# Kernel optimization log

Hardware: AMD Instinct MI355X
Metric: run time of the kernel (lower is better)

The kernel has to match this reference:

```python
import jax, jax.numpy as jnp
import numpy as np

B, HH, WW, D, NH, DK, DV, RATIO = 16, 48, 48, 512, 8, 64, 64, 3
EPS = 1e-5

def setup_inputs() -> dict:
    key = jax.random.key(0)
    ks = jax.random.split(key, 12)
    nq = HH * WW
    w = lambda i, shape: jax.random.normal(ks[i], shape, jnp.float32) * 0.02
    return {
        "queries": jax.random.normal(ks[0], (B, nq, D), jnp.float32),
        "Wq": w(1, (D, NH * DK)), "bq": jnp.zeros((NH * DK,), jnp.float32),
        "Wk": w(2, (D, NH * DK)), "bk": jnp.zeros((NH * DK,), jnp.float32),
        "Wv": w(3, (D, NH * DV)), "bv": jnp.zeros((NH * DV,), jnp.float32),
        "Wo": w(4, (NH * DV, D)), "bo": jnp.zeros((D,), jnp.float32),
        "sr_w": w(5, (D, 1, RATIO + 1, RATIO + 1)),  # depthwise conv, OIHW with I=1
        "sr_b": jnp.zeros((D,), jnp.float32),
        "ln_g": jnp.ones((D,), jnp.float32), "ln_b": jnp.zeros((D,), jnp.float32),
        "tw": w(6, (NH, NH)),  # 1x1 conv over head dim
        "tb": jnp.zeros((NH,), jnp.float32),
    }


def reference(queries, Wq, bq, Wk, bk, Wv, bv, Wo, bo, sr_w, sr_b, ln_g, ln_b, tw, tb):
    b, nq, c = queries.shape
    # Q projection -> (b, h, nq, d_k)
    q = (queries @ Wq + bq).reshape(b, nq, NH, DK).transpose(0, 2, 1, 3)
    # spatial reduction: depthwise strided conv over (H, W)
    x = queries.transpose(0, 2, 1).reshape(b, c, HH, WW)
    pad = RATIO // 2
    x = jax.lax.conv_general_dilated(
        x, sr_w, window_strides=(RATIO, RATIO),
        padding=[(pad, pad), (pad, pad)], feature_group_count=c,
        dimension_numbers=("NCHW", "OIHW", "NCHW"))
    x = x + sr_b[None, :, None, None]
    nk = x.shape[2] * x.shape[3]
    x = x.reshape(b, c, nk).transpose(0, 2, 1)  # (b, nk, c)
    # LayerNorm over channel dim
    mu = x.mean(-1, keepdims=True)
    var = x.var(-1, keepdims=True)
    x = (x - mu) / jnp.sqrt(var + EPS) * ln_g + ln_b
    # K, V projections
    k = (x @ Wk + bk).reshape(b, nk, NH, DK).transpose(0, 2, 3, 1)  # (b,h,d_k,nk)
    v = (x @ Wv + bv).reshape(b, nk, NH, DV).transpose(0, 2, 1, 3)  # (b,h,nk,d_v)
    # scaled attention scores
    att = jnp.einsum("bhqd,bhdk->bhqk", q, k) / jnp.sqrt(jnp.float32(DK))
    # transform: 1x1 conv over heads -> softmax(-1) -> InstanceNorm2d (no affine)
    att = jnp.einsum("oi,biqk->boqk", tw, att) + tb[None, :, None, None]
    att = jax.nn.softmax(att, axis=-1)
    m = att.mean((2, 3), keepdims=True)
    va = att.var((2, 3), keepdims=True)
    att = (att - m) / jnp.sqrt(va + EPS)
    # apply to values and output projection
    out = jnp.einsum("bhqk,bhkd->bhqd", att, v).transpose(0, 2, 1, 3).reshape(b, nq, NH * DV)
    return out @ Wo + bo
```

## Files before the change

kernel.cpp:

```cpp
#include <hip/hip_runtime.h>
#include <hip/hip_bf16.h>
#include <stdint.h>


typedef __bf16 bf16;
typedef __bf16 bf16x4 __attribute__((ext_vector_type(4)));
typedef __bf16 bf16x8 __attribute__((ext_vector_type(8)));
typedef float  f32x4  __attribute__((ext_vector_type(4)));

#define LDS_AS  __attribute__((address_space(3)))
#define GLOB_AS __attribute__((address_space(1)))

__device__ __forceinline__ void gload_lds16(const bf16* g, void* l) {
    __builtin_amdgcn_global_load_lds((const GLOB_AS void*)g, (LDS_AS void*)l, 16, 0, 0);
}

#define NB   16
#define NQ   2304
#define DD   512
#define NKV  256

constexpr size_t OFF_WQT = 0;
constexpr size_t OFF_WKT = 512*512*2;
constexpr size_t OFF_WVT = 2*512*512*2;
constexpr size_t OFF_WOT = 3*512*512*2;
constexpr size_t OFF_X   = 4*512*512*2;
constexpr size_t OFF_KT  = OFF_X  + 4194304;
constexpr size_t OFF_VT  = OFF_KT + 4194304;
constexpr size_t OFF_SS  = OFF_VT + 4194304;
constexpr size_t OFF_SM  = OFF_SS + 512;
constexpr size_t OFF_TWF = OFF_SM + 24064;
constexpr size_t OFF_FLG = OFF_TWF + 256;
constexpr size_t OFF_QF  = OFF_FLG + 256;
constexpr size_t OFF_U   = OFF_QF + (size_t)NB*NQ*DD*2;
constexpr size_t OFF_S   = OFF_U  + (size_t)NB*NQ*DD*2;
constexpr size_t SPLANE  = (size_t)NQ*NKV*2;
constexpr size_t OFF_WOTP = OFF_X;

#define SM_BQ  0
#define SM_BK  512
#define SM_BV  1024
#define SM_BO  1536
#define SM_SRW 2048
#define SM_SRB 10240
#define SM_LNG 10752
#define SM_LNB 11264
#define SM_TW  11776

__global__ __launch_bounds__(64) void detect_dtype(const uint32_t* __restrict__ q,
                                                   int* __restrict__ flag)
{
    int t = threadIdx.x;
    int cnt = 0;
    #pragma unroll
    for (int i = 0; i < 8; i++) {
        uint32_t w = q[t*8 + i];
        int e = (w >> 7) & 0xFF;
        cnt += (e >= 100 && e <= 150) ? 1 : 0;
    }
    #pragma unroll
    for (int m = 1; m < 64; m <<= 1) cnt += __shfl_xor(cnt, m);
    if (t == 0) *flag = (cnt >= 384) ? 0 : 1;
}

__global__ __launch_bounds__(256) void convert_q(const void* __restrict__ in,
                                                 bf16* __restrict__ out,
                                                 const int* __restrict__ flag)
{
    if (*flag == 0) return;
    int idx = blockIdx.x * 256 + threadIdx.x;
    f32x4 a = ((const f32x4*)in)[(size_t)idx*2];
    f32x4 b = ((const f32x4*)in)[(size_t)idx*2 + 1];
    bf16x8 r;
    #pragma unroll
    for (int i = 0; i < 4; i++) { r[i] = (bf16)a[i]; r[i+4] = (bf16)b[i]; }
    ((bf16x8*)out)[idx] = r;
}

__global__ __launch_bounds__(256) void convert_small(
    const void* s0, const void* s1, const void* s2, const void* s3,
    const void* s4, const void* s5, const void* s6, const void* s7,
    const void* s8, bf16* __restrict__ dst, float* __restrict__ twf,
    const int* __restrict__ flag)
{
    const void* srcs[9] = {s0,s1,s2,s3,s4,s5,s6,s7,s8};
    const int sizes[9]  = {512,512,512,512,8192,512,512,512,64};
    const int offs[9]   = {SM_BQ,SM_BK,SM_BV,SM_BO,SM_SRW,SM_SRB,SM_LNG,SM_LNB,SM_TW};
    const float scl[9]  = {0.125f,1.f,1.f,1.f,1.f,1.f,1.f,1.f,1.f};
    int b = blockIdx.x;
    const void* s = srcs[b];
    int n = sizes[b], o = offs[b];
    float sc = scl[b];
    bool f32 = (*flag != 0);
    for (int i = threadIdx.x; i < n; i += 256) {
        float v = f32 ? ((const float*)s)[i] : (float)((const bf16*)s)[i];
        dst[o + i] = (bf16)(v * sc);
        if (b == 8) twf[i] = v;
    }
}

__global__ __launch_bounds__(256) void transpose512(
    const void* s0, const void* s1, const void* s2, const void* s3,
    bf16* __restrict__ d0, bf16* __restrict__ d1,
    bf16* __restrict__ d2, bf16* __restrict__ d3,
    const int* __restrict__ flag)
{
    __shared__ bf16 tile[32][33];
    bool f32 = (*flag != 0);
    int wsel = blockIdx.z;
    const void* src = wsel == 0 ? s0 : wsel == 1 ? s1 : wsel == 2 ? s2 : s3;
    bf16*       dst = wsel == 0 ? d0 : wsel == 1 ? d1 : wsel == 2 ? d2 : d3;
    float scl = (wsel == 0) ? 0.125f : 1.0f;
    int c0 = blockIdx.x * 32, n0 = blockIdx.y * 32;
    int tx = threadIdx.x, ty = threadIdx.y;
    #pragma unroll
    for (int i = 0; i < 4; i++) {
        size_t idx = (size_t)(c0 + ty + i*8) * 512 + n0 + tx;
        float v = f32 ? ((const float*)src)[idx] : (float)((const bf16*)src)[idx];
        tile[ty + i*8][tx] = (bf16)(v * scl);
    }
    __syncthreads();
    #pragma unroll
    for (int i = 0; i < 4; i++)
        dst[(size_t)(n0 + ty + i*8) * 512 + c0 + tx] = tile[tx][ty + i*8];
}

__global__ __launch_bounds__(256) void sr_ln(
    const void* __restrict__ qraw, const bf16* __restrict__ qc,
    const bf16* __restrict__ sm, bf16* __restrict__ x,
    const int* __restrict__ flag)
{
    const bf16* q = (*flag) ? qc : (const bf16*)qraw;
    const bf16* srw  = sm + SM_SRW;
    const bf16* srb  = sm + SM_SRB;
    const bf16* g    = sm + SM_LNG;
    const bf16* beta = sm + SM_LNB;
    int bo = blockIdx.x;
    int b  = bo >> 8, ok = bo & 255;
    int oh = ok >> 4, ow = ok & 15;
    int t  = threadIdx.x;

    float v[2];
    #pragma unroll
    for (int h = 0; h < 2; h++) {
        int ch = t + h*256;
        float acc = 0.f;
        #pragma unroll
        for (int kh = 0; kh < 4; kh++) {
            int ih = oh*3 - 1 + kh;
            if (ih < 0) continue;
            #pragma unroll
            for (int kw = 0; kw < 4; kw++) {
                int iw = ow*3 - 1 + kw;
                if (iw < 0) continue;
                acc += (float)q[((size_t)b*NQ + ih*48 + iw)*DD + ch]
                     * (float)srw[ch*16 + kh*4 + kw];
            }
        }
        v[h] = acc + (float)srb[ch];
    }
    float s = v[0] + v[1], s2 = v[0]*v[0] + v[1]*v[1];
    #pragma unroll
    for (int m = 1; m < 64; m <<= 1) { s += __shfl_xor(s, m); s2 += __shfl_xor(s2, m); }
    __shared__ float ps[4], ps2[4];
    if ((t & 63) == 0) { ps[t >> 6] = s; ps2[t >> 6] = s2; }
    __syncthreads();
    s  = ps[0] + ps[1] + ps[2] + ps[3];
    s2 = ps2[0] + ps2[1] + ps2[2] + ps2[3];
    float mu  = s * (1.f/512.f);
    float var = s2 * (1.f/512.f) - mu*mu;
    float inv = rsqrtf(var + 1e-5f);
    #pragma unroll
    for (int h = 0; h < 2; h++) {
        int ch = t + h*256;
        float y = (v[h] - mu) * inv * (float)g[ch] + (float)beta[ch];
        x[(size_t)bo * DD + ch] = (bf16)y;
    }
}

template <int MODE>
__global__ __launch_bounds__(256) void gemm_bt(
    const bf16* __restrict__ A, const bf16* __restrict__ Bt,
    const bf16* __restrict__ bias, bf16* __restrict__ C,
    const int* __restrict__ of32, const bf16* __restrict__ A2)
{
    constexpr int K = 512;
    __shared__ bf16 Al[128 * 64];
    __shared__ bf16 Bl[128 * 64];
    const int m0 = blockIdx.x * 128, n0 = blockIdx.y * 128;
    const int t = threadIdx.x;
    const int lane = t & 63, w = t >> 6;
    const int wr = w >> 1, wc = w & 1;
    const int gg = lane >> 4, li = lane & 15;
    const int fsw = (li & 7) << 4;
    bool f32o = false;
    if (MODE == 2) f32o = (*of32 != 0);

    const bf16* Ab = A;
    if (MODE == 4) Ab = (*of32) ? A2 : A;
    const bf16* Btb = Bt;
    if (MODE == 2) Btb = Bt + (size_t)(m0 / 2304) * (512 * 512);

    f32x4 acc[4][4] = {};

    for (int k0 = 0; k0 < K; k0 += 64) {
        #pragma unroll
        for (int p = 0; p < 4; p++) {
            int off = p*4096 + t*16;
            int row = off >> 7;
            int col = ((((off >> 4) & 7) ^ (row & 7)) << 3);
            gload_lds16(Ab + (size_t)(m0 + row)*K + k0 + col, (char*)Al + off);
        }
        #pragma unroll
        for (int p = 0; p < 4; p++) {
            int off = p*4096 + t*16;
            int row = off >> 7;
            int col = ((((off >> 4) & 7) ^ (row & 7)) << 3);
            gload_lds16(Btb + (size_t)(n0 + row)*K + k0 + col, (char*)Bl + off);
        }
        __syncthreads();
        #pragma unroll
        for (int kk = 0; kk < 2; kk++) {
            bf16x8 af[4], bfr[4];
            #pragma unroll
            for (int i = 0; i < 4; i++) {
                af[i]  = *(const bf16x8*)((char*)Al + (wr*64 + i*16 + li)*128 + ((kk*64 + gg*16) ^ fsw));
                bfr[i] = *(const bf16x8*)((char*)Bl + (wc*64 + i*16 + li)*128 + ((kk*64 + gg*16) ^ fsw));
            }
            __builtin_amdgcn_s_setprio(1);
            #pragma unroll
            for (int i = 0; i < 4; i++)
                #pragma unroll
                for (int j = 0; j < 4; j++)
                    acc[i][j] = __builtin_amdgcn_mfma_f32_16x16x32_bf16(af[i], bfr[j], acc[i][j], 0, 0, 0);
            __builtin_amdgcn_s_setprio(0);
        }
        __syncthreads();
    }

    #pragma unroll
    for (int i = 0; i < 4; i++) {
        #pragma unroll
        for (int j = 0; j < 4; j++) {
            int rbase = m0 + wr*64 + i*16 + gg*4;
            int c     = n0 + wc*64 + j*16 + li;
            float bv = (float)bias[c];
            #pragma unroll
            for (int jj = 0; jj < 4; jj++) {
                float val = acc[i][j][jj] + bv;
                int r = rbase + jj;
                if (MODE == 1) {
                    int bb = r >> 8, kk2 = r & 255;
                    int hh = c >> 6, dv = c & 63;
                    C[(((size_t)(bb*8 + hh))*64 + dv)*256 + kk2] = (bf16)val;
                } else if (MODE == 2) {
                    if (f32o) ((float*)C)[(size_t)r * 512 + c] = val;
                    else      C[(size_t)r * 512 + c] = (bf16)val;
                } else {
                    C[(size_t)r * 512 + c] = (bf16)val;
                }
            }
        }
    }
}

__global__ __launch_bounds__(256) void gemm_s(
    const bf16* __restrict__ Qf, const bf16* __restrict__ Kt, bf16* __restrict__ S,
    int b0)
{
    __shared__ bf16 Al[128 * 64];
    __shared__ bf16 Bl[128 * 64];
    const int m0 = blockIdx.x * 128, n0 = blockIdx.y * 128;
    const int bo = blockIdx.z;
    const int b = b0 + (bo >> 3), ih = bo & 7;
    const int t = threadIdx.x;
    const int lane = t & 63, w = t >> 6;
    const int wr = w >> 1, wc = w & 1;
    const int gg = lane >> 4, li = lane & 15;
    const int fsw = (li & 7) << 4;

    #pragma unroll
    for (int p = 0; p < 4; p++) {
        int off = p*4096 + t*16;
        int row = off >> 7;
        int col = ((((off >> 4) & 7) ^ (row & 7)) << 3);
        gload_lds16(Qf + ((size_t)(b*NQ + m0 + row))*DD + ih*64 + col, (char*)Al + off);
    }
    #pragma unroll
    for (int p = 0; p < 4; p++) {
        int off = p*4096 + t*16;
        int row = off >> 7;
        int col = ((((off >> 4) & 7) ^ (row & 7)) << 3);
        gload_lds16(Kt + ((size_t)(b*NKV + n0 + row))*DD + ih*64 + col, (char*)Bl + off);
    }
    __syncthreads();

    f32x4 acc[4][4] = {};
    #pragma unroll
    for (int kk = 0; kk < 2; kk++) {
        bf16x8 af[4], bfr[4];
        #pragma unroll
        for (int i = 0; i < 4; i++) {
            af[i]  = *(const bf16x8*)((char*)Al + (wr*64 + i*16 + li)*128 + ((kk*64 + gg*16) ^ fsw));
            bfr[i] = *(const bf16x8*)((char*)Bl + (wc*64 + i*16 + li)*128 + ((kk*64 + gg*16) ^ fsw));
        }
        __builtin_amdgcn_s_setprio(1);
        #pragma unroll
        for (int i = 0; i < 4; i++)
            #pragma unroll
            for (int j = 0; j < 4; j++)
                acc[i][j] = __builtin_amdgcn_mfma_f32_16x16x32_bf16(af[i], bfr[j], acc[i][j], 0, 0, 0);
        __builtin_amdgcn_s_setprio(0);
    }

    bf16* Sb = S + (size_t)bo * NQ * NKV;
    #pragma unroll
    for (int i = 0; i < 4; i++) {
        #pragma unroll
        for (int j = 0; j < 4; j++) {
            int rbase = m0 + wr*64 + i*16 + gg*4;
            int c     = n0 + wc*64 + j*16 + li;
            #pragma unroll
            for (int jj = 0; jj < 4; jj++)
                Sb[(size_t)(rbase + jj) * NKV + c] = (bf16)acc[i][j][jj];
        }
    }
}

__global__ __launch_bounds__(256) void mix_softmax(
    bf16* __restrict__ S, const float* __restrict__ twf,
    float* __restrict__ ssq_g, int b0)
{
    const int t = threadIdx.x;
    const int lane = t & 63, w = t >> 6;
    const int bl = blockIdx.y;
    const int b  = b0 + bl;
    const int q0 = blockIdx.x * 32 + w * 8;
    __shared__ float rpar[4][8];

    float tw[8][8];
    #pragma unroll
    for (int o = 0; o < 8; o++)
        #pragma unroll
        for (int i = 0; i < 8; i++)
            tw[o][i] = twf[o*8 + i];

    float ssqL[8] = {};
    for (int qi = 0; qi < 8; qi++) {
        float s[8][4];
        #pragma unroll
        for (int i = 0; i < 8; i++) {
            bf16x4 v = *(const bf16x4*)(S + (((size_t)(bl*8 + i))*NQ + (q0 + qi))*NKV + lane*4);
            #pragma unroll
            for (int r = 0; r < 4; r++) s[i][r] = (float)v[r];
        }
        float e[8][4], inv[8];
        #pragma unroll
        for (int o = 0; o < 8; o++) {
            float sum = 0.f;
            #pragma unroll
            for (int r = 0; r < 4; r++) {
                float a = 0.f;
                #pragma unroll
                for (int i = 0; i < 8; i++) a += tw[o][i] * s[i][r];
                a = fminf(fmaxf(a, -30.f), 30.f);
                e[o][r] = __expf(a);
                sum += e[o][r];
            }
            #pragma unroll
            for (int m = 1; m < 64; m <<= 1) sum += __shfl_xor(sum, m);
            inv[o] = 1.0f / sum;
        }
        #pragma unroll
        for (int o = 0; o < 8; o++) {
            bf16x4 dv;
            #pragma unroll
            for (int r = 0; r < 4; r++) {
                float d = e[o][r] * inv[o] - (1.0f/256.0f);
                ssqL[o] += d * d;
                dv[r] = (bf16)d;
            }
            *(bf16x4*)(S + (((size_t)(bl*8 + o))*NQ + (q0 + qi))*NKV + lane*4) = dv;
        }
    }
    #pragma unroll
    for (int o = 0; o < 8; o++) {
        float s = ssqL[o];
        #pragma unroll
        for (int m = 1; m < 64; m <<= 1) s += __shfl_xor(s, m);
        if (lane == 0) rpar[w][o] = s;
    }
    __syncthreads();
    if (t < 8) {
        float tot = rpar[0][t] + rpar[1][t] + rpar[2][t] + rpar[3][t];
        atomicAdd(&ssq_g[b*8 + t], tot);
    }
}

__global__ __launch_bounds__(256) void gemm_pv(
    const bf16* __restrict__ Dev, const bf16* __restrict__ VT, bf16* __restrict__ U,
    int b0)
{
    __shared__ bf16 Al[128 * 64];
    __shared__ bf16 Bl[64 * 64];
    const int m0 = blockIdx.x * 128;
    const int bo = blockIdx.y;
    const int b = b0 + (bo >> 3), o = bo & 7;
    const int t = threadIdx.x;
    const int lane = t & 63, w = t >> 6;
    const int wr = w >> 1, wc = w & 1;
    const int gg = lane >> 4, li = lane & 15;
    const int fsw = (li & 7) << 4;

    const bf16* Ab = Dev + (size_t)bo * NQ * NKV;
    const bf16* Bb = VT + ((size_t)(b*8 + o)) * 64 * NKV;

    f32x4 acc[4][2] = {};

    for (int k0 = 0; k0 < 256; k0 += 64) {
        #pragma unroll
        for (int p = 0; p < 4; p++) {
            int off = p*4096 + t*16;
            int row = off >> 7;
            int col = ((((off >> 4) & 7) ^ (row & 7)) << 3);
            gload_lds16(Ab + (size_t)(m0 + row)*NKV + k0 + col, (char*)Al + off);
        }
        #pragma unroll
        for (int p = 0; p < 2; p++) {
            int off = p*4096 + t*16;
            int row = off >> 7;
            int col = ((((off >> 4) & 7) ^ (row & 7)) << 3);
            gload_lds16(Bb + (size_t)row*NKV + k0 + col, (char*)Bl + off);
        }
        __syncthreads();
        #pragma unroll
        for (int kk = 0; kk < 2; kk++) {
            bf16x8 af[4], bfr[2];
            #pragma unroll
            for (int i = 0; i < 4; i++)
                af[i] = *(const bf16x8*)((char*)Al + (wr*64 + i*16 + li)*128 + ((kk*64 + gg*16) ^ fsw));
            #pragma unroll
            for (int j = 0; j < 2; j++)
                bfr[j] = *(const bf16x8*)((char*)Bl + (wc*32 + j*16 + li)*128 + ((kk*64 + gg*16) ^ fsw));
            __builtin_amdgcn_s_setprio(1);
            #pragma unroll
            for (int i = 0; i < 4; i++)
                #pragma unroll
                for (int j = 0; j < 2; j++)
                    acc[i][j] = __builtin_amdgcn_mfma_f32_16x16x32_bf16(af[i], bfr[j], acc[i][j], 0, 0, 0);
            __builtin_amdgcn_s_setprio(0);
        }
        __syncthreads();
    }

    #pragma unroll
    for (int i = 0; i < 4; i++) {
        #pragma unroll
        for (int j = 0; j < 2; j++) {
            int rbase = m0 + wr*64 + i*16 + gg*4;
            int c = wc*32 + j*16 + li;
            #pragma unroll
            for (int jj = 0; jj < 4; jj++)
                U[((size_t)b*NQ + rbase + jj)*DD + o*64 + c] = (bf16)acc[i][j][jj];
        }
    }
}

__global__ __launch_bounds__(256) void scale_wot(const bf16* __restrict__ WoT,
                                                 const float* __restrict__ ssq,
                                                 bf16* __restrict__ out)
{
    int idx = blockIdx.x * 256 + threadIdx.x;
    int c8 = idx & 63;
    int c  = (idx >> 6) & 511;
    int b  = idx >> 15;
    int h  = c8 >> 3;
    float va = ssq[b*8 + h] * (1.0f / ((float)NQ * (float)NKV));
    float s  = rsqrtf(va + 1e-5f);
    bf16x8 v = *(const bf16x8*)(WoT + ((size_t)c << 9) + c8*8);
    bf16x8 r;
    #pragma unroll
    for (int i = 0; i < 8; i++) r[i] = (bf16)((float)v[i] * s);
    *(bf16x8*)(out + ((size_t)idx << 3)) = r;
}

extern "C" void kernel_launch(void* const* d_in, const int* in_sizes, int n_in,
                              void* d_out, int out_size, void* d_ws, size_t ws_size,
                              hipStream_t stream)
{
    const void* queries = d_in[0];
    const void* Wq = d_in[1];  const void* bq = d_in[2];
    const void* Wk = d_in[3];  const void* bk = d_in[4];
    const void* Wv = d_in[5];  const void* bv = d_in[6];
    const void* Wo = d_in[7];  const void* bo = d_in[8];
    const void* srw = d_in[9]; const void* srb = d_in[10];
    const void* lng = d_in[11]; const void* lnb = d_in[12];
    const void* tw  = d_in[13];

    char* ws = (char*)d_ws;
    bf16* WqT = (bf16*)(ws + OFF_WQT);
    bf16* WkT = (bf16*)(ws + OFF_WKT);
    bf16* WvT = (bf16*)(ws + OFF_WVT);
    bf16* WoT = (bf16*)(ws + OFF_WOT);
    bf16* xb  = (bf16*)(ws + OFF_X);
    bf16* Kt  = (bf16*)(ws + OFF_KT);
    bf16* VTb = (bf16*)(ws + OFF_VT);
    bf16* Qf  = (bf16*)(ws + OFF_QF);
    bf16* Ub  = (bf16*)(ws + OFF_U);
    float* ss = (float*)(ws + OFF_SS);
    bf16* sm  = (bf16*)(ws + OFF_SM);
    float* twf = (float*)(ws + OFF_TWF);
    int* flag = (int*)(ws + OFF_FLG);
    bf16* WoTp = (bf16*)(ws + OFF_WOTP);
    bf16* Sb  = (bf16*)(ws + OFF_S);
    bf16* Qc  = Ub;

    int CB = 1;
    if      (OFF_S + 16*8*SPLANE <= ws_size) CB = 16;
    else if (OFF_S +  8*8*SPLANE <= ws_size) CB = 8;
    else if (OFF_S +  4*8*SPLANE <= ws_size) CB = 4;
    else if (OFF_S +  2*8*SPLANE <= ws_size) CB = 2;

    detect_dtype<<<dim3(1), dim3(64), 0, stream>>>((const uint32_t*)queries, flag);
    hipMemsetAsync(ss, 0, 128 * sizeof(float), stream);

    convert_q<<<dim3(9216), dim3(256), 0, stream>>>(queries, Qc, flag);
    convert_small<<<dim3(9), dim3(256), 0, stream>>>(bq, bk, bv, bo, srw, srb, lng, lnb, tw, sm, twf, flag);
    transpose512<<<dim3(16, 16, 4), dim3(32, 8), 0, stream>>>(Wq, Wk, Wv, Wo, WqT, WkT, WvT, WoT, flag);

    sr_ln<<<dim3(NB * NKV), dim3(256), 0, stream>>>(queries, Qc, sm, xb, flag);
    gemm_bt<0><<<dim3(32, 4), dim3(256), 0, stream>>>(xb, WkT, sm + SM_BK, Kt, nullptr, nullptr);
    gemm_bt<1><<<dim3(32, 4), dim3(256), 0, stream>>>(xb, WvT, sm + SM_BV, VTb, nullptr, nullptr);
    gemm_bt<4><<<dim3(288, 4), dim3(256), 0, stream>>>((const bf16*)queries, WqT, sm + SM_BQ, Qf, flag, Qc);

    for (int b0 = 0; b0 < NB; b0 += CB) {
        gemm_s<<<dim3(18, 2, CB*8), dim3(256), 0, stream>>>(Qf, Kt, Sb, b0);
        mix_softmax<<<dim3(72, CB), dim3(256), 0, stream>>>(Sb, twf, ss, b0);
        gemm_pv<<<dim3(18, CB*8), dim3(256), 0, stream>>>(Sb, VTb, Ub, b0);
    }

    scale_wot<<<dim3(2048), dim3(256), 0, stream>>>(WoT, ss, WoTp);
    gemm_bt<2><<<dim3(288, 4), dim3(256), 0, stream>>>(Ub, WoTp, sm + SM_BO, (bf16*)d_out, flag, nullptr);
}
```

Before: 337.8 us.

## Fuse QK^T score GEMM with head-mixing softmax into one kernel

Merges the per-head score GEMM and the head-mixing softmax kernel into a single kernel. Each 512-thread block computes all 8 heads' scores for 16 queries in registers, then applies the 8x8 head mix, softmax and deviation write directly. This removes the bf16 write and re-read of the full score tensor between the two kernels. In exchange, K tiles are reloaded per head for every 16-query block and the exponentials are computed twice. Each block also now does only a small MFMA tile per head, which may leave the matrix units underused.

Result: slower. 414.5 us (+22.7%).

```diff
diff --git a/kernel.cpp b/kernel.cpp
--- a/kernel.cpp
+++ b/kernel.cpp
@@ -264,123 +264,105 @@
     }
 }
 
-__global__ __launch_bounds__(256) void gemm_s(
-    const bf16* __restrict__ Qf, const bf16* __restrict__ Kt, bf16* __restrict__ S,
-    int b0)
-{
-    __shared__ bf16 Al[128 * 64];
-    __shared__ bf16 Bl[128 * 64];
-    const int m0 = blockIdx.x * 128, n0 = blockIdx.y * 128;
-    const int bo = blockIdx.z;
-    const int b = b0 + (bo >> 3), ih = bo & 7;
+__global__ __launch_bounds__(512, 2) void gemm_s_mix(
+    const bf16* __restrict__ Qf, const bf16* __restrict__ Kt,
+    const float* __restrict__ twf, bf16* __restrict__ Dev,
+    float* __restrict__ ssq_g, int b0)
+{
+    __shared__ bf16 Ql[16 * 512];
+    __shared__ bf16 Kl[256 * 64];
+    __shared__ float srow[8 * 16 * 8];
+    __shared__ float rpar[8][8];
+
     const int t = threadIdx.x;
     const int lane = t & 63, w = t >> 6;
-    const int wr = w >> 1, wc = w & 1;
     const int gg = lane >> 4, li = lane & 15;
-    const int fsw = (li & 7) << 4;
-
-    #pragma unroll
-    for (int p = 0; p < 4; p++) {
-        int off = p*4096 + t*16;
-        int row = off >> 7;
-        int col = ((((off >> 4) & 7) ^ (row & 7)) << 3);
-        gload_lds16(Qf + ((size_t)(b*NQ + m0 + row))*DD + ih*64 + col, (char*)Al + off);
-    }
-    #pragma unroll
-    for (int p = 0; p < 4; p++) {
-        int off = p*4096 + t*16;
-        int row = off >> 7;
-        int col = ((((off >> 4) & 7) ^ (row & 7)) << 3);
-        gload_lds16(Kt + ((size_t)(b*NKV + n0 + row))*DD + ih*64 + col, (char*)Bl + off);
-    }
-    __syncthreads();
-
-    f32x4 acc[4][4] = {};
-    #pragma unroll
-    for (int kk = 0; kk < 2; kk++) {
-        bf16x8 af[4], bfr[4];
-        #pragma unroll
-        for (int i = 0; i < 4; i++) {
-            af[i]  = *(const bf16x8*)((char*)Al + (wr*64 + i*16 + li)*128 + ((kk*64 + gg*16) ^ fsw));
-            bfr[i] = *(const bf16x8*)((char*)Bl + (wc*64 + i*16 + li)*128 + ((kk*64 + gg*16) ^ fsw));
-        }
-        __builtin_amdgcn_s_setprio(1);
-        #pragma unroll
-        for (int i = 0; i < 4; i++)
-            #pragma unroll
-            for (int j = 0; j < 4; j++)
-                acc[i][j] = __builtin_amdgcn_mfma_f32_16x16x32_bf16(af[i], bfr[j], acc[i][j], 0, 0, 0);
-        __builtin_amdgcn_s_setprio(0);
-    }
-
-    bf16* Sb = S + (size_t)bo * NQ * NKV;
-    #pragma unroll
-    for (int i = 0; i < 4; i++) {
-        #pragma unroll
-        for (int j = 0; j < 4; j++) {
-            int rbase = m0 + wr*64 + i*16 + gg*4;
-            int c     = n0 + wc*64 + j*16 + li;
-            #pragma unroll
-            for (int jj = 0; jj < 4; jj++)
-                Sb[(size_t)(rbase + jj) * NKV + c] = (bf16)acc[i][j][jj];
-        }
-    }
-}
-
-__global__ __launch_bounds__(256) void mix_softmax(
-    bf16* __restrict__ S, const float* __restrict__ twf,
-    float* __restrict__ ssq_g, int b0)
-{
-    const int t = threadIdx.x;
-    const int lane = t & 63, w = t >> 6;
     const int bl = blockIdx.y;
     const int b  = b0 + bl;
-    const int q0 = blockIdx.x * 32 + w * 8;
-    __shared__ float rpar[4][8];
-
-    float tw[8][8];
-    #pragma unroll
-    for (int o = 0; o < 8; o++)
-        #pragma unroll
-        for (int i = 0; i < 8; i++)
-            tw[o][i] = twf[o*8 + i];
-
-    float ssqL[8] = {};
-    for (int qi = 0; qi < 8; qi++) {
-        float s[8][4];
-        #pragma unroll
-        for (int i = 0; i < 8; i++) {
-            bf16x4 v = *(const bf16x4*)(S + (((size_t)(bl*8 + i))*NQ + (q0 + qi))*NKV + lane*4);
-            #pragma unroll
-            for (int r = 0; r < 4; r++) s[i][r] = (float)v[r];
-        }
-        float e[8][4], inv[8];
-        #pragma unroll
-        for (int o = 0; o < 8; o++) {
-            float sum = 0.f;
-            #pragma unroll
-            for (int r = 0; r < 4; r++) {
+    const int q0 = blockIdx.x * 16;
+
+    #pragma unroll
+    for (int p = 0; p < 2; p++) {
+        int off = p*8192 + t*16;
+        int q = off >> 10, slot = (off >> 4) & 63;
+        gload_lds16(Qf + ((size_t)(b*NQ + q0 + q))*DD + ((slot ^ (q & 7)) << 3),
+                    (char*)Ql + off);
+    }
+
+    f32x4 acc[8][2] = {};
+
+    for (int i = 0; i < 8; i++) {
+        if (i > 0) __syncthreads();
+        #pragma unroll
+        for (int p = 0; p < 4; p++) {
+            int off = p*8192 + t*16;
+            int kr = off >> 7, slot = (off >> 4) & 7;
+            gload_lds16(Kt + ((size_t)(b*NKV + kr))*DD + i*64 + ((slot ^ (kr & 7)) << 3),
+                        (char*)Kl + off);
+        }
+        __syncthreads();
+        #pragma unroll
+        for (int kk = 0; kk < 2; kk++) {
+            bf16x8 af = *(const bf16x8*)((char*)Ql + li*1024
+                          + ((i*128 + kk*64 + gg*16) ^ ((li & 7) << 4)));
+            #pragma unroll
+            for (int nt = 0; nt < 2; nt++) {
+                int kr = w*32 + nt*16 + li;
+                bf16x8 bfr = *(const bf16x8*)((char*)Kl + kr*128
+                               + ((kk*64 + gg*16) ^ ((kr & 7) << 4)));
+                acc[i][nt] = __builtin_amdgcn_mfma_f32_16x16x32_bf16(af, bfr, acc[i][nt], 0, 0, 0);
+            }
+        }
+    }
+
+    #pragma unroll
+    for (int o = 0; o < 8; o++) {
+        float two[8];
+        #pragma unroll
+        for (int i = 0; i < 8; i++) two[i] = twf[o*8 + i];
+        #pragma unroll
+        for (int r = 0; r < 4; r++) {
+            float s = 0.f;
+            #pragma unroll
+            for (int nt = 0; nt < 2; nt++) {
                 float a = 0.f;
                 #pragma unroll
-                for (int i = 0; i < 8; i++) a += tw[o][i] * s[i][r];
+                for (int i = 0; i < 8; i++) a += two[i] * acc[i][nt][r];
                 a = fminf(fmaxf(a, -30.f), 30.f);
-                e[o][r] = __expf(a);
-                sum += e[o][r];
+                s += __expf(a);
             }
-            #pragma unroll
-            for (int m = 1; m < 64; m <<= 1) sum += __shfl_xor(sum, m);
-            inv[o] = 1.0f / sum;
-        }
-        #pragma unroll
-        for (int o = 0; o < 8; o++) {
-            bf16x4 dv;
-            #pragma unroll
-            for (int r = 0; r < 4; r++) {
-                float d = e[o][r] * inv[o] - (1.0f/256.0f);
+            s += __shfl_xor(s, 1); s += __shfl_xor(s, 2);
+            s += __shfl_xor(s, 4); s += __shfl_xor(s, 8);
+            if (li == 0) srow[(o*16 + gg*4 + r)*8 + w] = s;
+        }
+    }
+    __syncthreads();
+
+    float ssqL[8];
+    #pragma unroll
+    for (int o = 0; o < 8; o++) ssqL[o] = 0.f;
+    #pragma unroll
+    for (int o = 0; o < 8; o++) {
+        float two[8];
+        #pragma unroll
+        for (int i = 0; i < 8; i++) two[i] = twf[o*8 + i];
+        bf16* Dp = Dev + ((size_t)(bl*8 + o))*NQ*NKV;
+        #pragma unroll
+        for (int r = 0; r < 4; r++) {
+            int q = gg*4 + r;
+            f32x4 s0 = *(const f32x4*)&srow[(o*16 + q)*8];
+            f32x4 s1 = *(const f32x4*)&srow[(o*16 + q)*8 + 4];
+            float inv = 1.0f / (s0[0]+s0[1]+s0[2]+s0[3]+s1[0]+s1[1]+s1[2]+s1[3]);
+            #pragma unroll
+            for (int nt = 0; nt < 2; nt++) {
+                float a = 0.f;
+                #pragma unroll
+                for (int i = 0; i < 8; i++) a += two[i] * acc[i][nt][r];
+                a = fminf(fmaxf(a, -30.f), 30.f);
+                float d = __expf(a) * inv - (1.0f/256.0f);
                 ssqL[o] += d * d;
-                dv[r] = (bf16)d;
+                Dp[(size_t)(q0 + q)*NKV + w*32 + nt*16 + li] = (bf16)d;
             }
-            *(bf16x4*)(S + (((size_t)(bl*8 + o))*NQ + (q0 + qi))*NKV + lane*4) = dv;
         }
     }
     #pragma unroll
@@ -392,7 +374,9 @@
     }
     __syncthreads();
     if (t < 8) {
-        float tot = rpar[0][t] + rpar[1][t] + rpar[2][t] + rpar[3][t];
+        float tot = 0.f;
+        #pragma unroll
+        for (int i = 0; i < 8; i++) tot += rpar[i][t];
         atomicAdd(&ssq_g[b*8 + t], tot);
     }
 }
@@ -534,8 +518,7 @@
     gemm_bt<4><<<dim3(288, 4), dim3(256), 0, stream>>>((const bf16*)queries, WqT, sm + SM_BQ, Qf, flag, Qc);
 
     for (int b0 = 0; b0 < NB; b0 += CB) {
-        gemm_s<<<dim3(18, 2, CB*8), dim3(256), 0, stream>>>(Qf, Kt, Sb, b0);
-        mix_softmax<<<dim3(72, CB), dim3(256), 0, stream>>>(Sb, twf, ss, b0);
+        gemm_s_mix<<<dim3(144, CB), dim3(512), 0, stream>>>(Qf, Kt, twf, Sb, ss, b0);
         gemm_pv<<<dim3(18, CB*8), dim3(256), 0, stream>>>(Sb, VTb, Ub, b0);
     }
 
```
